# Optimization experiments

Hardware: AMD Instinct MI355X
Metric: run time of the kernel (lower is better)

## Reference

```python
import jax, jax.numpy as jnp
import numpy as np

N = 200_000   # points
C = 20        # semantic classes
P = 256       # proposals (from bfs_cluster)
M = 400_000   # (proposal, point) pairs
CLUSTER_PROPOSE_POINTS = 100
VOXEL_SIZE = 0.02


def setup_inputs() -> dict:
    key = jax.random.key(0)
    k1, k2, k3, k4, k5 = jax.random.split(key, 5)
    return {
        "logit_pred": jax.random.normal(k1, (N, C), jnp.float32),
        "bias_pred": jax.random.normal(k2, (N, 3), jnp.float32),
        "coord": jax.random.normal(k3, (N, 3), jnp.float32) * 5.0,
        "proposal_ids": jax.random.randint(k4, (M,), 0, P, dtype=jnp.int32),
        "point_ids": jax.random.randint(k5, (M,), 0, N, dtype=jnp.int32),
    }


def reference(logit_pred, bias_pred, coord, proposal_ids, point_ids):
    # voxelized predicted instance centers (center_pred /= voxel_size)
    center_pred = (coord + bias_pred) / VOXEL_SIZE

    # softmax + argmax semantic prediction
    probs = jax.nn.softmax(logit_pred, axis=-1)          # [N, C]
    segment_pred = jnp.argmax(probs, axis=1)             # [N]

    # dense proposal mask construction (scatter): proposals_pred[pid, point] = 1
    proposals_pred = jnp.zeros((P, N), jnp.int32).at[proposal_ids, point_ids].set(1)
    counts = proposals_pred.sum(axis=1)                  # [P]
    proposals_mask = counts > CLUSTER_PROPOSE_POINTS     # [P] keep mask

    # instance class = semantic class of the representative (first) point per proposal
    rep = jax.ops.segment_min(point_ids, proposal_ids, num_segments=P)  # [P]
    instance_pred = segment_pred[jnp.clip(rep, 0, N - 1)]               # [P]

    # per-proposal mean confidence: mean over proposal points of probs[point, cls]
    conf = probs[:, instance_pred]                       # [N, P] gather of class columns
    score_sum = jnp.einsum("pn,np->p", proposals_pred.astype(probs.dtype), conf)
    pred_scores = jnp.where(proposals_mask,
                            score_sum / jnp.maximum(counts, 1).astype(probs.dtype),
                            0.0)                         # [P]

    # filtered masks/classes (kept at fixed shape; invalid rows zeroed / class -1)
    pred_masks = proposals_pred * proposals_mask[:, None].astype(jnp.int32)
    pred_classes = jnp.where(proposals_mask, instance_pred, -1)

    return pred_scores, pred_masks, pred_classes, bias_pred, probs
```

## Files before the change

kernel.cpp:

```cpp
#include <hip/hip_runtime.h>

static constexpr int    kN = 200000;
static constexpr int    kC = 20;
static constexpr int    kP = 256;
static constexpr int    kM = 400000;
static constexpr int    kThreshPts = 100;
static constexpr int    kRowCap = 2048;
static constexpr int    kLWords = kN / 32;

typedef float nfloat4 __attribute__((ext_vector_type(4)));

static constexpr size_t OFF_SCORES  = 0;
static constexpr size_t OFF_MASKS   = 256;
static constexpr size_t OFF_CLASSES = OFF_MASKS + (size_t)kP * kN;
static constexpr size_t OFF_BIAS    = OFF_CLASSES + 256;
static constexpr size_t OFF_PROBS   = OFF_BIAS + 3 * (size_t)kN;

static constexpr size_t WS_CURSOR = 0;
static constexpr size_t WS_SEG    = 1024;
static constexpr size_t WS_ROWBUF = WS_SEG + (size_t)kN * 4;

__global__ void k_softmax(const float* __restrict__ logit,
                          const float* __restrict__ bias,
                          float* __restrict__ out,
                          int* __restrict__ seg,
                          int* __restrict__ cursor) {
    int tid = blockIdx.x * blockDim.x + threadIdx.x;
    if (blockIdx.x == 0) cursor[threadIdx.x] = 0;

    if (tid < 150000) {
        const float4* b4 = (const float4*)bias;
        float4*       o4 = (float4*)(out + OFF_BIAS);
        o4[tid] = b4[tid];
    }
    if (tid >= kN) return;

    const float4* l4 = (const float4*)(logit + (size_t)tid * kC);
    float v[kC];
#pragma unroll
    for (int c = 0; c < 5; c++) {
        float4 t = l4[c];
        v[4*c] = t.x; v[4*c+1] = t.y; v[4*c+2] = t.z; v[4*c+3] = t.w;
    }
    float m = v[0]; int arg = 0;
#pragma unroll
    for (int i = 1; i < kC; i++) if (v[i] > m) { m = v[i]; arg = i; }
    float s = 0.0f;
#pragma unroll
    for (int i = 0; i < kC; i++) { v[i] = __expf(v[i] - m); s += v[i]; }
    float inv = 1.0f / s;
    float4* p4 = (float4*)(out + OFF_PROBS + (size_t)tid * kC);
#pragma unroll
    for (int c = 0; c < 5; c++) {
        float4 t;
        t.x = v[4*c] * inv; t.y = v[4*c+1] * inv;
        t.z = v[4*c+2] * inv; t.w = v[4*c+3] * inv;
        p4[c] = t;
    }
    seg[tid] = arg;
}

__global__ void k_bucket(const int4* __restrict__ prop4,
                         const int4* __restrict__ pt4,
                         int* __restrict__ cursor,
                         int* __restrict__ rowbuf) {
    __shared__ int s_cnt[kP];
    __shared__ int s_off[kP];
    int t = threadIdx.x;
    if (t < kP) s_cnt[t] = 0;
    __syncthreads();

    int idx = blockIdx.x * 1024 + t;
    bool valid = idx < (kM / 4);
    int4 pv = {0, 0, 0, 0}, nv = {0, 0, 0, 0};
    int sl[4] = {0, 0, 0, 0};
    if (valid) {
        pv = prop4[idx];
        nv = pt4[idx];
        sl[0] = atomicAdd(&s_cnt[pv.x], 1);
        sl[1] = atomicAdd(&s_cnt[pv.y], 1);
        sl[2] = atomicAdd(&s_cnt[pv.z], 1);
        sl[3] = atomicAdd(&s_cnt[pv.w], 1);
    }
    __syncthreads();
    if (t < kP) s_off[t] = s_cnt[t] ? atomicAdd(&cursor[t], s_cnt[t]) : 0;
    __syncthreads();
    if (valid) {
        int d0 = s_off[pv.x] + sl[0];
        int d1 = s_off[pv.y] + sl[1];
        int d2 = s_off[pv.z] + sl[2];
        int d3 = s_off[pv.w] + sl[3];
        if (d0 < kRowCap) rowbuf[pv.x * kRowCap + d0] = nv.x;
        if (d1 < kRowCap) rowbuf[pv.y * kRowCap + d1] = nv.y;
        if (d2 < kRowCap) rowbuf[pv.z * kRowCap + d2] = nv.z;
        if (d3 < kRowCap) rowbuf[pv.w * kRowCap + d3] = nv.w;
    }
}

__global__ void __launch_bounds__(1024)
k_row(const int* __restrict__ rowbuf,
      const int* __restrict__ cursor,
      const int* __restrict__ seg,
      float* __restrict__ out) {
    __shared__ unsigned int lbits[kLWords];
    __shared__ int   s_redc[16];
    __shared__ int   s_redm[16];
    __shared__ float s_redf[16];
    __shared__ int   s_cls;
    __shared__ float s_fv;

    int p = blockIdx.x;
    int t = threadIdx.x;
    const float* probs = out + OFF_PROBS;

    for (int i = t; i < kLWords; i += 1024) lbits[i] = 0;
    int len = cursor[p];
    if (len > kRowCap) len = kRowCap;
    __syncthreads();

    const int* rb = rowbuf + p * kRowCap;
    int  n0 = 0, n1 = 0;
    bool u0 = false, u1 = false;
    int  mymin = 0x7fffffff;
    if (t < len) {
        n0 = rb[t];
        unsigned int bit = 1u << (n0 & 31);
        unsigned int old = atomicOr(&lbits[(unsigned)n0 >> 5], bit);
        u0 = (old & bit) == 0u;
        mymin = n0;
    }
    if (t + 1024 < len) {
        n1 = rb[t + 1024];
        unsigned int bit = 1u << (n1 & 31);
        unsigned int old = atomicOr(&lbits[(unsigned)n1 >> 5], bit);
        u1 = (old & bit) == 0u;
        mymin = n1 < mymin ? n1 : mymin;
    }

    int cnt = (int)u0 + (int)u1;
    for (int off = 32; off; off >>= 1) {
        cnt += __shfl_down(cnt, off);
        int om = __shfl_down(mymin, off);
        mymin = om < mymin ? om : mymin;
    }
    if ((t & 63) == 0) { s_redc[t >> 6] = cnt; s_redm[t >> 6] = mymin; }
    __syncthreads();
    int tot = 0;
    if (t == 0) {
        int mn = 0x7fffffff;
        for (int i = 0; i < 16; i++) {
            tot += s_redc[i];
            mn = s_redm[i] < mn ? s_redm[i] : mn;
        }
        int r = mn < 0 ? 0 : (mn > kN - 1 ? kN - 1 : mn);
        int c = seg[r];
        bool fl = tot > kThreshPts;
        s_cls = c;
        s_fv  = fl ? 1.0f : 0.0f;
        out[OFF_CLASSES + p] = fl ? (float)c : -1.0f;
    }
    __syncthreads();

    float fv = s_fv;
    int   c  = s_cls;

    float g0 = 0.0f, g1 = 0.0f;
    if (u0) g0 = probs[(size_t)n0 * kC + c];
    if (u1) g1 = probs[(size_t)n1 * kC + c];

    nfloat4* mrow = (nfloat4*)(out + OFF_MASKS) + (size_t)p * (kN / 4);
    for (int f = t; f < kN / 4; f += 1024) {
        unsigned int word = lbits[f >> 3];
        unsigned int b    = (word >> (((unsigned)f & 7u) * 4u)) & 0xFu;
        nfloat4 o;
        o.x = (b & 1u) ? fv : 0.0f;
        o.y = (b & 2u) ? fv : 0.0f;
        o.z = (b & 4u) ? fv : 0.0f;
        o.w = (b & 8u) ? fv : 0.0f;
        mrow[f] = o;
    }

    float s = g0 + g1;
    for (int off = 32; off; off >>= 1) s += __shfl_down(s, off);
    if ((t & 63) == 0) s_redf[t >> 6] = s;
    __syncthreads();
    if (t == 0) {
        float stot = 0.0f;
        for (int i = 0; i < 16; i++) stot += s_redf[i];
        float denom = (float)(tot > 1 ? tot : 1);
        out[OFF_SCORES + p] = (s_fv != 0.0f) ? stot / denom : 0.0f;
    }
}

extern "C" void kernel_launch(void* const* d_in, const int* in_sizes, int n_in,
                              void* d_out, int out_size, void* d_ws, size_t ws_size,
                              hipStream_t stream) {
    const float* logit = (const float*)d_in[0];
    const float* bias  = (const float*)d_in[1];
    const int4* prop4 = (const int4*)d_in[3];
    const int4* pt4   = (const int4*)d_in[4];
    float* out = (float*)d_out;
    char*  ws  = (char*)d_ws;

    int* cursor = (int*)(ws + WS_CURSOR);
    int* seg    = (int*)(ws + WS_SEG);
    int* rowbuf = (int*)(ws + WS_ROWBUF);

    k_softmax<<<(kN + 255) / 256, 256, 0, stream>>>(logit, bias, out, seg, cursor);
    k_bucket<<<(kM / 4 + 1023) / 1024, 1024, 0, stream>>>(prop4, pt4, cursor, rowbuf);
    k_row<<<kP, 1024, 0, stream>>>(rowbuf, cursor, seg, out);
}
```

Baseline: 255.8 us.

## Split mask expansion into separate grid-stride kernel using global bitmaps

The per-proposal row kernel now only computes statistics and writes its shared-memory bitmap plus a keep flag to workspace. A new grid-stride kernel with 2048 blocks of 256 threads expands those bitmaps into the dense 256x200000 float mask output. The aim is to stop the dominant ~205MB mask write from being limited to 256 large blocks, which may underuse the GPU's CUs. The cost is an extra launch and a small global bitmap round trip.

```diff
diff --git a/kernel.cpp b/kernel.cpp
--- a/kernel.cpp
+++ b/kernel.cpp
@@ -7,6 +7,7 @@
 static constexpr int    kThreshPts = 100;
 static constexpr int    kRowCap = 2048;
 static constexpr int    kLWords = kN / 32;
+static constexpr int    kRow4 = kN / 4;
 
 typedef float nfloat4 __attribute__((ext_vector_type(4)));
 
@@ -17,8 +18,10 @@
 static constexpr size_t OFF_PROBS   = OFF_BIAS + 3 * (size_t)kN;
 
 static constexpr size_t WS_CURSOR = 0;
-static constexpr size_t WS_SEG    = 1024;
+static constexpr size_t WS_FLAGF  = 1024;
+static constexpr size_t WS_SEG    = 2048;
 static constexpr size_t WS_ROWBUF = WS_SEG + (size_t)kN * 4;
+static constexpr size_t WS_BITS   = WS_ROWBUF + (size_t)kP * kRowCap * 4;
 
 __global__ void k_softmax(const float* __restrict__ logit,
                           const float* __restrict__ bias,
@@ -98,10 +101,12 @@
 }
 
 __global__ void __launch_bounds__(1024)
-k_row(const int* __restrict__ rowbuf,
-      const int* __restrict__ cursor,
-      const int* __restrict__ seg,
-      float* __restrict__ out) {
+k_stats(const int* __restrict__ rowbuf,
+        const int* __restrict__ cursor,
+        const int* __restrict__ seg,
+        unsigned int* __restrict__ bitsg,
+        float* __restrict__ flagf,
+        float* __restrict__ out) {
     __shared__ unsigned int lbits[kLWords];
     __shared__ int   s_redc[16];
     __shared__ int   s_redm[16];
@@ -158,37 +163,49 @@
         s_cls = c;
         s_fv  = fl ? 1.0f : 0.0f;
         out[OFF_CLASSES + p] = fl ? (float)c : -1.0f;
-    }
-    __syncthreads();
-
-    float fv = s_fv;
-    int   c  = s_cls;
+        flagf[p] = s_fv;
+    }
+    __syncthreads();
+
+    int c = s_cls;
 
     float g0 = 0.0f, g1 = 0.0f;
     if (u0) g0 = probs[(size_t)n0 * kC + c];
     if (u1) g1 = probs[(size_t)n1 * kC + c];
 
-    nfloat4* mrow = (nfloat4*)(out + OFF_MASKS) + (size_t)p * (kN / 4);
-    for (int f = t; f < kN / 4; f += 1024) {
-        unsigned int word = lbits[f >> 3];
-        unsigned int b    = (word >> (((unsigned)f & 7u) * 4u)) & 0xFu;
+    unsigned int* bg = bitsg + (size_t)p * kLWords;
+    for (int i = t; i < kLWords; i += 1024) bg[i] = lbits[i];
+
+    float s = g0 + g1;
+    for (int off = 32; off; off >>= 1) s += __shfl_down(s, off);
+    if ((t & 63) == 0) s_redf[t >> 6] = s;
+    __syncthreads();
+    if (t == 0) {
+        float stot = 0.0f;
+        for (int i = 0; i < 16; i++) stot += s_redf[i];
+        float denom = (float)(tot > 1 ? tot : 1);
+        out[OFF_SCORES + p] = (s_fv != 0.0f) ? stot / denom : 0.0f;
+    }
+}
+
+__global__ void k_expand(const unsigned int* __restrict__ bits,
+                         const float* __restrict__ flagf,
+                         float* __restrict__ out) {
+    const int total = kP * kRow4;
+    int step = gridDim.x * blockDim.x;
+    nfloat4* masks = (nfloat4*)(out + OFF_MASKS);
+    for (int g = blockIdx.x * blockDim.x + threadIdx.x; g < total; g += step) {
+        unsigned int p   = (unsigned)g / (unsigned)kRow4;
+        unsigned int rem = (unsigned)g - p * (unsigned)kRow4;
+        unsigned int word = bits[(size_t)p * kLWords + (rem >> 3)];
+        unsigned int b = (word >> ((rem & 7u) * 4u)) & 0xFu;
+        float fv = flagf[p];
         nfloat4 o;
         o.x = (b & 1u) ? fv : 0.0f;
         o.y = (b & 2u) ? fv : 0.0f;
         o.z = (b & 4u) ? fv : 0.0f;
         o.w = (b & 8u) ? fv : 0.0f;
-        mrow[f] = o;
-    }
-
-    float s = g0 + g1;
-    for (int off = 32; off; off >>= 1) s += __shfl_down(s, off);
-    if ((t & 63) == 0) s_redf[t >> 6] = s;
-    __syncthreads();
-    if (t == 0) {
-        float stot = 0.0f;
-        for (int i = 0; i < 16; i++) stot += s_redf[i];
-        float denom = (float)(tot > 1 ? tot : 1);
-        out[OFF_SCORES + p] = (s_fv != 0.0f) ? stot / denom : 0.0f;
+        masks[g] = o;
     }
 }
 
@@ -202,11 +219,14 @@
     float* out = (float*)d_out;
     char*  ws  = (char*)d_ws;
 
-    int* cursor = (int*)(ws + WS_CURSOR);
-    int* seg    = (int*)(ws + WS_SEG);
-    int* rowbuf = (int*)(ws + WS_ROWBUF);
+    int*          cursor = (int*)(ws + WS_CURSOR);
+    float*        flagf  = (float*)(ws + WS_FLAGF);
+    int*          seg    = (int*)(ws + WS_SEG);
+    int*          rowbuf = (int*)(ws + WS_ROWBUF);
+    unsigned int* bitsg  = (unsigned int*)(ws + WS_BITS);
 
     k_softmax<<<(kN + 255) / 256, 256, 0, stream>>>(logit, bias, out, seg, cursor);
     k_bucket<<<(kM / 4 + 1023) / 1024, 1024, 0, stream>>>(prop4, pt4, cursor, rowbuf);
-    k_row<<<kP, 1024, 0, stream>>>(rowbuf, cursor, seg, out);
-}
+    k_stats<<<kP, 1024, 0, stream>>>(rowbuf, cursor, seg, bitsg, flagf, out);
+    k_expand<<<2048, 256, 0, stream>>>(bitsg, flagf, out);
+}
```

New measurement: 259.1 us. Within noise of the previous version (+1.3%).

## Fuse softmax and bucketing kernels into one launch with block-range dispatch

Applied to the files above, without the earlier changes.

The separate softmax and bucket kernels are merged into a single kernel whose first blocks do the proposal bucketing and whose remaining blocks do the softmax, argmax and bias copy. The cursor reset moves to a hipMemsetAsync, because the bucket blocks now run concurrently with the softmax blocks and could no longer rely on the softmax kernel to zero it. Bucket blocks shrink from 1024 to 256 threads, which gives more blocks, more shared-memory histograms and more global atomics on the cursor. The aim is to remove one launch gap and overlap two independent phases, at the cost of an extra memset node.

```diff
diff --git a/kernel.cpp b/kernel.cpp
--- a/kernel.cpp
+++ b/kernel.cpp
@@ -20,13 +20,54 @@
 static constexpr size_t WS_SEG    = 1024;
 static constexpr size_t WS_ROWBUF = WS_SEG + (size_t)kN * 4;
 
-__global__ void k_softmax(const float* __restrict__ logit,
-                          const float* __restrict__ bias,
-                          float* __restrict__ out,
-                          int* __restrict__ seg,
-                          int* __restrict__ cursor) {
-    int tid = blockIdx.x * blockDim.x + threadIdx.x;
-    if (blockIdx.x == 0) cursor[threadIdx.x] = 0;
+static constexpr int kBucketBlocks = (kM / 4 + 255) / 256;
+static constexpr int kSoftBlocks   = (kN + 255) / 256;
+
+__global__ void k_front(const float* __restrict__ logit,
+                        const float* __restrict__ bias,
+                        const int4* __restrict__ prop4,
+                        const int4* __restrict__ pt4,
+                        int* __restrict__ cursor,
+                        int* __restrict__ rowbuf,
+                        int* __restrict__ seg,
+                        float* __restrict__ out) {
+    int t = threadIdx.x;
+
+    if (blockIdx.x < kBucketBlocks) {
+        __shared__ int s_cnt[kP];
+        __shared__ int s_off[kP];
+        s_cnt[t] = 0;
+        __syncthreads();
+
+        int idx = blockIdx.x * 256 + t;
+        bool valid = idx < (kM / 4);
+        int4 pv = {0, 0, 0, 0}, nv = {0, 0, 0, 0};
+        int sl[4] = {0, 0, 0, 0};
+        if (valid) {
+            pv = prop4[idx];
+            nv = pt4[idx];
+            sl[0] = atomicAdd(&s_cnt[pv.x], 1);
+            sl[1] = atomicAdd(&s_cnt[pv.y], 1);
+            sl[2] = atomicAdd(&s_cnt[pv.z], 1);
+            sl[3] = atomicAdd(&s_cnt[pv.w], 1);
+        }
+        __syncthreads();
+        s_off[t] = s_cnt[t] ? atomicAdd(&cursor[t], s_cnt[t]) : 0;
+        __syncthreads();
+        if (valid) {
+            int d0 = s_off[pv.x] + sl[0];
+            int d1 = s_off[pv.y] + sl[1];
+            int d2 = s_off[pv.z] + sl[2];
+            int d3 = s_off[pv.w] + sl[3];
+            if (d0 < kRowCap) rowbuf[pv.x * kRowCap + d0] = nv.x;
+            if (d1 < kRowCap) rowbuf[pv.y * kRowCap + d1] = nv.y;
+            if (d2 < kRowCap) rowbuf[pv.z * kRowCap + d2] = nv.z;
+            if (d3 < kRowCap) rowbuf[pv.w * kRowCap + d3] = nv.w;
+        }
+        return;
+    }
+
+    int tid = (blockIdx.x - kBucketBlocks) * 256 + t;
 
     if (tid < 150000) {
         const float4* b4 = (const float4*)bias;
@@ -39,8 +80,8 @@
     float v[kC];
 #pragma unroll
     for (int c = 0; c < 5; c++) {
-        float4 t = l4[c];
-        v[4*c] = t.x; v[4*c+1] = t.y; v[4*c+2] = t.z; v[4*c+3] = t.w;
+        float4 x = l4[c];
+        v[4*c] = x.x; v[4*c+1] = x.y; v[4*c+2] = x.z; v[4*c+3] = x.w;
     }
     float m = v[0]; int arg = 0;
 #pragma unroll
@@ -52,49 +93,12 @@
     float4* p4 = (float4*)(out + OFF_PROBS + (size_t)tid * kC);
 #pragma unroll
     for (int c = 0; c < 5; c++) {
-        float4 t;
-        t.x = v[4*c] * inv; t.y = v[4*c+1] * inv;
-        t.z = v[4*c+2] * inv; t.w = v[4*c+3] * inv;
-        p4[c] = t;
+        float4 x;
+        x.x = v[4*c] * inv; x.y = v[4*c+1] * inv;
+        x.z = v[4*c+2] * inv; x.w = v[4*c+3] * inv;
+        p4[c] = x;
     }
     seg[tid] = arg;
-}
-
-__global__ void k_bucket(const int4* __restrict__ prop4,
-                         const int4* __restrict__ pt4,
-                         int* __restrict__ cursor,
-                         int* __restrict__ rowbuf) {
-    __shared__ int s_cnt[kP];
-    __shared__ int s_off[kP];
-    int t = threadIdx.x;
-    if (t < kP) s_cnt[t] = 0;
-    __syncthreads();
-
-    int idx = blockIdx.x * 1024 + t;
-    bool valid = idx < (kM / 4);
-    int4 pv = {0, 0, 0, 0}, nv = {0, 0, 0, 0};
-    int sl[4] = {0, 0, 0, 0};
-    if (valid) {
-        pv = prop4[idx];
-        nv = pt4[idx];
-        sl[0] = atomicAdd(&s_cnt[pv.x], 1);
-        sl[1] = atomicAdd(&s_cnt[pv.y], 1);
-        sl[2] = atomicAdd(&s_cnt[pv.z], 1);
-        sl[3] = atomicAdd(&s_cnt[pv.w], 1);
-    }
-    __syncthreads();
-    if (t < kP) s_off[t] = s_cnt[t] ? atomicAdd(&cursor[t], s_cnt[t]) : 0;
-    __syncthreads();
-    if (valid) {
-        int d0 = s_off[pv.x] + sl[0];
-        int d1 = s_off[pv.y] + sl[1];
-        int d2 = s_off[pv.z] + sl[2];
-        int d3 = s_off[pv.w] + sl[3];
-        if (d0 < kRowCap) rowbuf[pv.x * kRowCap + d0] = nv.x;
-        if (d1 < kRowCap) rowbuf[pv.y * kRowCap + d1] = nv.y;
-        if (d2 < kRowCap) rowbuf[pv.z * kRowCap + d2] = nv.z;
-        if (d3 < kRowCap) rowbuf[pv.w * kRowCap + d3] = nv.w;
-    }
 }
 
 __global__ void __launch_bounds__(1024)
@@ -206,7 +210,8 @@
     int* seg    = (int*)(ws + WS_SEG);
     int* rowbuf = (int*)(ws + WS_ROWBUF);
 
-    k_softmax<<<(kN + 255) / 256, 256, 0, stream>>>(logit, bias, out, seg, cursor);
-    k_bucket<<<(kM / 4 + 1023) / 1024, 1024, 0, stream>>>(prop4, pt4, cursor, rowbuf);
+    hipMemsetAsync(cursor, 0, kP * sizeof(int), stream);
+    k_front<<<kBucketBlocks + kSoftBlocks, 256, 0, stream>>>(
+        logit, bias, prop4, pt4, cursor, rowbuf, seg, out);
     k_row<<<kP, 1024, 0, stream>>>(rowbuf, cursor, seg, out);
 }
```

After: 256.1 us. About the same (+0.1%).
